# Optimization experiments

Measured on AMD Instinct MI355X. Metric: run time of the kernel, lower is better.

The kernel has to match this reference:

```python
import jax, jax.numpy as jnp
import numpy as np

BETA = 0.25


def setup_inputs() -> dict:
    key = jax.random.key(0)
    k1, k2 = jax.random.split(key)
    B, T, D, K = 16, 4096, 256, 4096
    z_e = jax.random.normal(k1, (B, T, D), dtype=jnp.float32)
    # emulate uniform(-1/K, 1/K) init but any values work for correctness
    codebook = jax.random.uniform(k2, (K, D), dtype=jnp.float32,
                                  minval=-1.0 / K, maxval=1.0 / K)
    return {"z_e": z_e, "codebook": codebook}


def reference(z_e, codebook):
    D = codebook.shape[1]
    z_flat = z_e.reshape(-1, D)                                  # [N, D]
    # squared L2 distances: ||z||^2 + ||e||^2 - 2 z.e
    z_norm = jnp.sum(z_flat ** 2, axis=1, keepdims=True)          # [N, 1]
    e_norm = jnp.sum(codebook ** 2, axis=1)                       # [K]
    dist = z_norm + e_norm - 2.0 * jnp.matmul(z_flat, codebook.T) # [N, K]
    idx_flat = jnp.argmin(dist, axis=1)                           # [N]
    idx = idx_flat.reshape(z_e.shape[:-1])                        # [B, T]
    z_q = codebook[idx]                                           # [B, T, D]
    # commitment loss: beta * mse(stop_grad(z_q), z_e)
    loss = BETA * jnp.mean((jax.lax.stop_gradient(z_q) - z_e) ** 2)
    # straight-through estimator
    z_q_st = z_e + jax.lax.stop_gradient(z_q - z_e)
    return z_q_st, idx, loss
```

## Files before the change

kernel.cpp:

```cpp
#include <hip/hip_runtime.h>
#include <cfloat>

#define NROWS 65536
#define DIM   256
#define KCB   4096

#define EPS_WIN  1.8e-4f
#define CAND_CAP 16
#define SROWS    64

typedef __attribute__((ext_vector_type(8))) short short8;
typedef __attribute__((ext_vector_type(4))) float f32x4;

__device__ inline unsigned short f2bf(float x) {
  unsigned int u = __float_as_uint(x);
  return (unsigned short)((u + 0x7fffu + ((u >> 16) & 1u)) >> 16);
}

__global__ void prep_norms_kernel(const float* __restrict__ z, const float* __restrict__ cb,
                                  unsigned short* __restrict__ zh, unsigned short* __restrict__ eh,
                                  float* __restrict__ znorm, float* __restrict__ enorm) {
  const int r    = blockIdx.x * 4 + (threadIdx.x >> 6);
  const int lane = threadIdx.x & 63;
  const float* src; unsigned short* dst; float* nrm; int row;
  if (r < NROWS) { src = z;  dst = zh; nrm = znorm; row = r; }
  else           { src = cb; dst = eh; nrm = enorm; row = r - NROWS; }
  const float4 v = ((const float4*)(src + (size_t)row * DIM))[lane];
  union { unsigned short us[4]; uint2 u2; } o;
  o.us[0] = f2bf(v.x); o.us[1] = f2bf(v.y); o.us[2] = f2bf(v.z); o.us[3] = f2bf(v.w);
  *(uint2*)(dst + (size_t)row * DIM + lane * 4) = o.u2;
  float s = v.x * v.x + v.y * v.y + v.z * v.z + v.w * v.w;
  #pragma unroll
  for (int off = 32; off > 0; off >>= 1) s += __shfl_down(s, off);
  if (lane == 0) nrm[row] = s;
}

__launch_bounds__(256, 3)
__global__ void screen_kernel(const unsigned short* __restrict__ zh,
                              const unsigned short* __restrict__ eh,
                              const float* __restrict__ enorm,
                              unsigned int* __restrict__ counts,
                              unsigned short* __restrict__ cands) {
  __shared__ __align__(16) unsigned short a_s[8][SROWS][32];
  __shared__ __align__(16) unsigned short b_s[2][128][32];
  __shared__ float tilemin_s[2][SROWS];
  __shared__ unsigned int cnt_s[SROWS];
  __shared__ unsigned short cand_s[SROWS * CAND_CAP];

  const int tid = threadIdx.x;
  const int wv  = tid >> 6;
  const int ln  = tid & 63;
  const int l15 = ln & 15;
  const int lg  = ln >> 4;
  const int wr  = wv >> 1;
  const int wc  = wv & 1;
  const int rbase = blockIdx.x * SROWS;

  if (tid < SROWS) cnt_s[tid] = 0u;

  {
    const unsigned short* abase = zh + (size_t)rbase * DIM;
    unsigned short* aflat = &a_s[0][0][0];
    #pragma unroll
    for (int i = 0; i < 8; ++i) {
      const int G  = i * 256 + tid;
      const int dc = G >> 8, rem = G & 255;
      const int c  = rem >> 2, sw = rem & 3;
      const int s4 = sw ^ ((c >> 1) & 3);
      __builtin_amdgcn_global_load_lds(
          (const uint4*)(abase + (size_t)c * 256 + dc * 32 + s4 * 8),
          (uint4*)(aflat + (size_t)G * 8), 16, 0, 0);
    }
  }

  float rm[8];
  #pragma unroll
  for (int s = 0; s < 8; ++s) rm[s] = FLT_MAX;

  unsigned short* bflat = &b_s[0][0][0];

  #pragma unroll 1
  for (int kt = 0; kt < KCB / 128; ++kt) {
    const int kcb0 = kt * 128;

    f32x4 acc[2][4];
    #pragma unroll
    for (int fr = 0; fr < 2; ++fr)
      #pragma unroll
      for (int fc = 0; fc < 4; ++fc)
        acc[fr][fc] = (f32x4){0.f, 0.f, 0.f, 0.f};

    #pragma unroll 1
    for (int ph = 0; ph < 4; ++ph) {
      __syncthreads();
      #pragma unroll
      for (int i = 0; i < 4; ++i) {
        const int G   = i * 256 + tid;
        const int dc2 = G >> 9, rem = G & 511;
        const int c   = rem >> 2, sw = rem & 3;
        const int s4  = sw ^ ((c >> 1) & 3);
        __builtin_amdgcn_global_load_lds(
            (const uint4*)(eh + (size_t)(kcb0 + c) * 256 + (ph * 2 + dc2) * 32 + s4 * 8),
            (uint4*)(bflat + (size_t)G * 8), 16, 0, 0);
      }
      __syncthreads();

      #pragma unroll
      for (int dc2 = 0; dc2 < 2; ++dc2) {
        const int dcg = ph * 2 + dc2;
        short8 af_[2];
        #pragma unroll
        for (int fr = 0; fr < 2; ++fr) {
          const int r  = wr * 32 + fr * 16 + l15;
          const int sl = lg ^ ((r >> 1) & 3);
          af_[fr] = *(const short8*)(&a_s[dcg][r][sl * 8]);
        }
        short8 bf[4];
        #pragma unroll
        for (int fc = 0; fc < 4; ++fc) {
          const int c  = wc * 64 + fc * 16 + l15;
          const int sw = lg ^ ((c >> 1) & 3);
          bf[fc] = *(const short8*)(&b_s[dc2][c][sw * 8]);
        }
        #pragma unroll
        for (int fr = 0; fr < 2; ++fr)
          #pragma unroll
          for (int fc = 0; fc < 4; ++fc)
            acc[fr][fc] = __builtin_amdgcn_mfma_f32_16x16x32_bf16(
                af_[fr], bf[fc], acc[fr][fc], 0, 0, 0);
      }
    }

    float en_[4];
    #pragma unroll
    for (int fc = 0; fc < 4; ++fc) en_[fc] = enorm[kcb0 + wc * 64 + fc * 16 + l15];

    float tm[8];
    #pragma unroll
    for (int s = 0; s < 8; ++s) tm[s] = FLT_MAX;

    #pragma unroll
    for (int fr = 0; fr < 2; ++fr)
      #pragma unroll
      for (int fc = 0; fc < 4; ++fc)
        #pragma unroll
        for (int q = 0; q < 4; ++q) {
          const float d_ = fmaf(-2.0f, acc[fr][fc][q], en_[fc]);
          tm[fr * 4 + q] = fminf(tm[fr * 4 + q], d_);
        }

    #pragma unroll
    for (int s = 0; s < 8; ++s) {
      float v = tm[s];
      v = fminf(v, __shfl_xor(v, 1));
      v = fminf(v, __shfl_xor(v, 2));
      v = fminf(v, __shfl_xor(v, 4));
      v = fminf(v, __shfl_xor(v, 8));
      if (l15 == 0)
        tilemin_s[wc][wr * 32 + (s >> 2) * 16 + lg * 4 + (s & 3)] = v;
    }
    __syncthreads();

    float gmin = FLT_MAX;
    #pragma unroll
    for (int s = 0; s < 8; ++s) {
      const int rl = wr * 32 + (s >> 2) * 16 + lg * 4 + (s & 3);
      const float comb = fminf(tilemin_s[0][rl], tilemin_s[1][rl]);
      const float m = fminf(rm[s], comb);
      rm[s] = m;
      gmin = fminf(gmin, tm[s] - m);
    }

    if (__any(gmin <= EPS_WIN)) {
      #pragma unroll
      for (int fr = 0; fr < 2; ++fr)
        #pragma unroll
        for (int fc = 0; fc < 4; ++fc)
          #pragma unroll
          for (int q = 0; q < 4; ++q) {
            const float d_ = fmaf(-2.0f, acc[fr][fc][q], en_[fc]);
            if (d_ <= rm[fr * 4 + q] + EPS_WIN) {
              const int rl = wr * 32 + fr * 16 + lg * 4 + q;
              const unsigned int pos = atomicAdd(&cnt_s[rl], 1u);
              if (pos < CAND_CAP)
                cand_s[rl * CAND_CAP + pos] =
                    (unsigned short)(kcb0 + wc * 64 + fc * 16 + l15);
            }
          }
    }
  }

  __syncthreads();
  if (tid < SROWS) counts[rbase + tid] = cnt_s[tid];
  for (int i = tid; i < SROWS * CAND_CAP; i += 256)
    cands[(size_t)rbase * CAND_CAP + i] = cand_s[i];
}

__global__ void rescore_kernel(const float* __restrict__ z, const float* __restrict__ cb,
                               const float* __restrict__ znorm, const float* __restrict__ enorm,
                               const unsigned int* __restrict__ counts,
                               const unsigned short* __restrict__ cands,
                               float* __restrict__ out_zq, float* __restrict__ out_idx,
                               float* __restrict__ partials) {
  const int gw  = (blockIdx.x * 256 + threadIdx.x) >> 6;
  const int ln  = threadIdx.x & 63;
  const int row = gw * 4 + (ln >> 4);
  const int ci  = ln & 15;
  const unsigned int cnt = counts[row];
  if (cnt > CAND_CAP) return;

  const int active = ci < (int)cnt;
  const int k = active ? (int)cands[(size_t)row * CAND_CAP + ci] : 0;
  const float4* zr4 = (const float4*)(z  + (size_t)row * DIM);
  const float4* er4 = (const float4*)(cb + (size_t)k   * DIM);
  float ax = 0.f, ay = 0.f, az = 0.f, aw = 0.f;
  #pragma unroll 4
  for (int d = 0; d < DIM / 4; ++d) {
    const float4 zv = zr4[d], ev = er4[d];
    ax = fmaf(zv.x, ev.x, ax); ay = fmaf(zv.y, ev.y, ay);
    az = fmaf(zv.z, ev.z, az); aw = fmaf(zv.w, ev.w, aw);
  }
  const float dot = (ax + ay) + (az + aw);
  const float dist = fmaf(-2.0f, dot, znorm[row] + enorm[k]);
  float bv = active ? dist : FLT_MAX;
  int   bk = active ? k : 0x7fffffff;
  #pragma unroll
  for (int off = 1; off < 16; off <<= 1) {
    const float ov = __shfl_xor(bv, off);
    const int   ok = __shfl_xor(bk, off);
    if (ov < bv || (ov == bv && ok < bk)) { bv = ov; bk = ok; }
  }
  const float4* br4 = (const float4*)(cb + (size_t)bk * DIM);
  float4* o4 = (float4*)(out_zq + (size_t)row * DIM);
  float sq = 0.0f;
  #pragma unroll
  for (int t = 0; t < 4; ++t) {
    const int p = ci + 16 * t;
    const float4 zv = zr4[p], ev = br4[p];
    float4 st;
    const float dx = ev.x - zv.x, dy = ev.y - zv.y, dz = ev.z - zv.z, dw = ev.w - zv.w;
    st.x = zv.x + dx; st.y = zv.y + dy; st.z = zv.z + dz; st.w = zv.w + dw;
    o4[p] = st;
    sq += dx * dx + dy * dy + dz * dz + dw * dw;
  }
  #pragma unroll
  for (int off = 1; off < 16; off <<= 1) sq += __shfl_xor(sq, off);
  if (ci == 0) { out_idx[row] = (float)bk; partials[row] = sq; }
}

__global__ void fallback_kernel(const float* __restrict__ z, const float* __restrict__ cb,
                                const float* __restrict__ znorm, const float* __restrict__ enorm,
                                const unsigned int* __restrict__ counts,
                                float* __restrict__ out_zq, float* __restrict__ out_idx,
                                float* __restrict__ partials) {
  __shared__ float bd_s[256];
  __shared__ int   bk_s[256];
  const int tid = threadIdx.x;
  for (int row = blockIdx.x; row < NROWS; row += gridDim.x) {
    if (counts[row] <= CAND_CAP) continue;
    const float zn = znorm[row];
    const float* zr = z + (size_t)row * DIM;
    float bv = FLT_MAX; int bk = 0x7fffffff;
    for (int k = tid; k < KCB; k += 256) {
      const float* er = cb + (size_t)k * DIM;
      float acc = 0.0f;
      #pragma unroll 8
      for (int d = 0; d < DIM; ++d) acc = fmaf(zr[d], er[d], acc);
      const float dist = fmaf(-2.0f, acc, zn + enorm[k]);
      if (dist < bv || (dist == bv && k < bk)) { bv = dist; bk = k; }
    }
    bd_s[tid] = bv; bk_s[tid] = bk;
    __syncthreads();
    for (int s = 128; s > 0; s >>= 1) {
      if (tid < s) {
        const float ov = bd_s[tid + s]; const int ok = bk_s[tid + s];
        if (ov < bd_s[tid] || (ov == bd_s[tid] && ok < bk_s[tid])) {
          bd_s[tid] = ov; bk_s[tid] = ok;
        }
      }
      __syncthreads();
    }
    const int kb = bk_s[0];
    const float zv = zr[tid];
    const float ev = cb[(size_t)kb * DIM + tid];
    const float dd = ev - zv;
    out_zq[(size_t)row * DIM + tid] = zv + dd;
    if (tid == 0) out_idx[row] = (float)kb;
    __syncthreads();
    bd_s[tid] = dd * dd;
    __syncthreads();
    for (int s = 128; s > 0; s >>= 1) {
      if (tid < s) bd_s[tid] += bd_s[tid + s];
      __syncthreads();
    }
    if (tid == 0) partials[row] = bd_s[0];
    __syncthreads();
  }
}

__global__ void loss_kernel(const float* __restrict__ partials, int n,
                            float* __restrict__ out_loss) {
  float s = 0.0f;
  for (int i = threadIdx.x; i < n; i += 256) s += partials[i];
  #pragma unroll
  for (int off = 32; off > 0; off >>= 1) s += __shfl_down(s, off);
  __shared__ float ps[4];
  if ((threadIdx.x & 63) == 0) ps[threadIdx.x >> 6] = s;
  __syncthreads();
  if (threadIdx.x == 0)
    *out_loss = 0.25f * (((ps[0] + ps[1]) + (ps[2] + ps[3])) *
                         (1.0f / (float)((size_t)NROWS * DIM)));
}

__global__ void norms_kernel(const float* __restrict__ x, float* __restrict__ out) {
  const int row  = blockIdx.x * 4 + (threadIdx.x >> 6);
  const int lane = threadIdx.x & 63;
  const float4 v = ((const float4*)(x + (size_t)row * DIM))[lane];
  float s = v.x * v.x + v.y * v.y + v.z * v.z + v.w * v.w;
  #pragma unroll
  for (int off = 32; off > 0; off >>= 1) s += __shfl_down(s, off);
  if (lane == 0) out[row] = s;
}

#define BM 128
#define BK 128
#define BD 32
#define LSTR 36
__launch_bounds__(256, 2)
__global__ void argmin_kernel(const float* __restrict__ z,
                              const float* __restrict__ cb,
                              const float* __restrict__ znorm,
                              const float* __restrict__ enorm,
                              int* __restrict__ idx_out) {
  __shared__ float z_s[BM * LSTR];
  __shared__ float e_s[BK * LSTR];
  __shared__ float zn_s[BM];
  const int tid = threadIdx.x;
  const int tx = tid & 15;
  const int ty = tid >> 4;
  const int rbase = blockIdx.x * BM;
  if (tid < BM) zn_s[tid] = znorm[rbase + tid];
  float bestv[8]; int besti[8];
  #pragma unroll
  for (int i = 0; i < 8; ++i) { bestv[i] = FLT_MAX; besti[i] = 0; }
  for (int kc = 0; kc < KCB; kc += BK) {
    float acc[8][8];
    #pragma unroll
    for (int i = 0; i < 8; ++i)
      #pragma unroll
      for (int j = 0; j < 8; ++j) acc[i][j] = 0.0f;
    for (int dc = 0; dc < DIM; dc += BD) {
      __syncthreads();
      #pragma unroll
      for (int p = 0; p < 4; ++p) {
        const int el = p * 256 + tid;
        const int r  = el >> 3;
        const int c4 = (el & 7) * 4;
        *(float4*)(&z_s[r * LSTR + c4]) =
            *(const float4*)(z + (size_t)(rbase + r) * DIM + dc + c4);
        *(float4*)(&e_s[r * LSTR + c4]) =
            *(const float4*)(cb + (size_t)(kc + r) * DIM + dc + c4);
      }
      __syncthreads();
      #pragma unroll 1
      for (int dd = 0; dd < BD; dd += 4) {
        float4 b[8];
        #pragma unroll
        for (int j = 0; j < 8; ++j)
          b[j] = *(const float4*)(&e_s[(tx + 16 * j) * LSTR + dd]);
        #pragma unroll
        for (int i = 0; i < 8; ++i) {
          const float4 a = *(const float4*)(&z_s[(ty + 16 * i) * LSTR + dd]);
          #pragma unroll
          for (int j = 0; j < 8; ++j)
            acc[i][j] += a.x * b[j].x + a.y * b[j].y + a.z * b[j].z + a.w * b[j].w;
        }
      }
    }
    float en[8];
    #pragma unroll
    for (int j = 0; j < 8; ++j) en[j] = enorm[kc + tx + 16 * j];
    #pragma unroll
    for (int i = 0; i < 8; ++i) {
      const float zn = zn_s[ty + 16 * i];
      #pragma unroll
      for (int j = 0; j < 8; ++j) {
        const float t1 = zn + en[j];
        const float dist = t1 - 2.0f * acc[i][j];
        const int k = kc + tx + 16 * j;
        if (dist < bestv[i]) { bestv[i] = dist; besti[i] = k; }
      }
    }
  }
  #pragma unroll
  for (int i = 0; i < 8; ++i) {
    float lv = bestv[i]; int li = besti[i];
    #pragma unroll
    for (int off = 1; off < 16; off <<= 1) {
      const float ov = __shfl_xor(lv, off);
      const int   oi = __shfl_xor(li, off);
      if (ov < lv || (ov == lv && oi < li)) { lv = ov; li = oi; }
    }
    if (tx == 0) idx_out[rbase + ty + 16 * i] = li;
  }
}

__global__ void gather_kernel(const float* __restrict__ z,
                              const float* __restrict__ cb,
                              const int* __restrict__ idx,
                              float* __restrict__ out_zq,
                              float* __restrict__ out_idx,
                              float* __restrict__ partials) {
  const int row  = blockIdx.x * 4 + (threadIdx.x >> 6);
  const int lane = threadIdx.x & 63;
  const int k = idx[row];
  const float4 zv = ((const float4*)(z  + (size_t)row * DIM))[lane];
  const float4 ev = ((const float4*)(cb + (size_t)k   * DIM))[lane];
  float4 d, st;
  d.x = ev.x - zv.x; d.y = ev.y - zv.y; d.z = ev.z - zv.z; d.w = ev.w - zv.w;
  st.x = zv.x + d.x; st.y = zv.y + d.y; st.z = zv.z + d.z; st.w = zv.w + d.w;
  ((float4*)(out_zq + (size_t)row * DIM))[lane] = st;
  if (lane == 0) out_idx[row] = (float)k;
  float s = d.x * d.x + d.y * d.y + d.z * d.z + d.w * d.w;
  #pragma unroll
  for (int off = 32; off > 0; off >>= 1) s += __shfl_down(s, off);
  __shared__ float ps[4];
  if (lane == 0) ps[threadIdx.x >> 6] = s;
  __syncthreads();
  if (threadIdx.x == 0)
    partials[blockIdx.x] = (ps[0] + ps[1]) + (ps[2] + ps[3]);
}

extern "C" void kernel_launch(void* const* d_in, const int* in_sizes, int n_in,
                              void* d_out, int out_size, void* d_ws, size_t ws_size,
                              hipStream_t stream) {
  const float* z  = (const float*)d_in[0];
  const float* cb = (const float*)d_in[1];

  float* out_zq   = (float*)d_out;
  float* out_idx  = out_zq + (size_t)NROWS * DIM;
  float* out_loss = out_idx + NROWS;

  char* w = (char*)d_ws;
  unsigned short* zh    = (unsigned short*)(w);
  unsigned short* eh    = (unsigned short*)(w + 33554432);
  float* enorm          = (float*)(w + 35651584);
  float* znorm          = (float*)(w + 35667968);
  unsigned int* counts  = (unsigned int*)(w + 36192256);
  unsigned short* cands = (unsigned short*)(w + 36454400);
  float* partials       = (float*)(w + 38551552);
  const size_t NEED = 38813696;

  if (ws_size >= NEED) {
    hipLaunchKernelGGL(prep_norms_kernel, dim3((NROWS + KCB) / 4), dim3(256), 0, stream,
                       z, cb, zh, eh, znorm, enorm);
    hipLaunchKernelGGL(screen_kernel, dim3(NROWS / SROWS), dim3(256), 0, stream,
                       zh, eh, enorm, counts, cands);
    hipLaunchKernelGGL(rescore_kernel, dim3(NROWS / 16), dim3(256), 0, stream,
                       z, cb, znorm, enorm, counts, cands, out_zq, out_idx, partials);
    hipLaunchKernelGGL(fallback_kernel, dim3(256), dim3(256), 0, stream,
                       z, cb, znorm, enorm, counts, out_zq, out_idx, partials);
    hipLaunchKernelGGL(loss_kernel, dim3(1), dim3(256), 0, stream,
                       partials, NROWS, out_loss);
  } else {
    float* ws         = (float*)d_ws;
    float* enorm_l    = ws;
    float* znorm_l    = ws + KCB;
    int*   idx_l      = (int*)(ws + KCB + NROWS);
    float* partials_l = ws + KCB + 2 * NROWS;
    hipLaunchKernelGGL(norms_kernel, dim3(KCB / 4), dim3(256), 0, stream, cb, enorm_l);
    hipLaunchKernelGGL(norms_kernel, dim3(NROWS / 4), dim3(256), 0, stream, z, znorm_l);
    hipLaunchKernelGGL(argmin_kernel, dim3(NROWS / BM), dim3(256), 0, stream,
                       z, cb, znorm_l, enorm_l, idx_l);
    hipLaunchKernelGGL(gather_kernel, dim3(NROWS / 4), dim3(256), 0, stream,
                       z, cb, idx_l, out_zq, out_idx, partials_l);
    hipLaunchKernelGGL(loss_kernel, dim3(1), dim3(256), 0, stream,
                       partials_l, NROWS / 4, out_loss);
  }
}
```

Before: 563.3 us.

## Double-buffer codebook tiles and give each wave full tile width

The screen kernel now double-buffers the codebook B tile in LDS. The next 32-dim chunk is prefetched with global_load_lds while MFMAs run on the current one, so there is one barrier per chunk instead of two per phase. Waves are remapped so each owns 16 rows across all 128 codebook columns, which removes the cross-wave shared-memory tile-min exchange and its extra barrier. In exchange, each wave reuses its A fragment across more B reads and issues more LDS reads of B per MFMA. The prefetch also wraps around and issues one redundant load at the end.

```diff
diff --git a/kernel.cpp b/kernel.cpp
--- a/kernel.cpp
+++ b/kernel.cpp
@@ -43,7 +43,6 @@
                               unsigned short* __restrict__ cands) {
   __shared__ __align__(16) unsigned short a_s[8][SROWS][32];
   __shared__ __align__(16) unsigned short b_s[2][128][32];
-  __shared__ float tilemin_s[2][SROWS];
   __shared__ unsigned int cnt_s[SROWS];
   __shared__ unsigned short cand_s[SROWS * CAND_CAP];
 
@@ -52,8 +51,6 @@
   const int ln  = tid & 63;
   const int l15 = ln & 15;
   const int lg  = ln >> 4;
-  const int wr  = wv >> 1;
-  const int wc  = wv & 1;
   const int rbase = blockIdx.x * SROWS;
 
   if (tid < SROWS) cnt_s[tid] = 0u;
@@ -71,122 +68,113 @@
           (const uint4*)(abase + (size_t)c * 256 + dc * 32 + s4 * 8),
           (uint4*)(aflat + (size_t)G * 8), 16, 0, 0);
     }
-  }
-
-  float rm[8];
-  #pragma unroll
-  for (int s = 0; s < 8; ++s) rm[s] = FLT_MAX;
-
-  unsigned short* bflat = &b_s[0][0][0];
+    unsigned short* b0 = &b_s[0][0][0];
+    #pragma unroll
+    for (int i = 0; i < 2; ++i) {
+      const int G  = i * 256 + tid;
+      const int c  = G >> 2, sw = G & 3;
+      const int s4 = sw ^ ((c >> 1) & 3);
+      __builtin_amdgcn_global_load_lds(
+          (const uint4*)(eh + (size_t)c * 256 + s4 * 8),
+          (uint4*)(b0 + (size_t)G * 8), 16, 0, 0);
+    }
+  }
+  __syncthreads();
+
+  const int ar = l15;
+  const int arow = wv * 16 + ar;
+  const int asl = lg ^ ((arow >> 1) & 3);
+
+  float rm[4];
+  #pragma unroll
+  for (int q = 0; q < 4; ++q) rm[q] = FLT_MAX;
+
+  int cur = 0;
 
   #pragma unroll 1
   for (int kt = 0; kt < KCB / 128; ++kt) {
     const int kcb0 = kt * 128;
 
-    f32x4 acc[2][4];
-    #pragma unroll
-    for (int fr = 0; fr < 2; ++fr)
-      #pragma unroll
-      for (int fc = 0; fc < 4; ++fc)
-        acc[fr][fc] = (f32x4){0.f, 0.f, 0.f, 0.f};
+    f32x4 acc[8];
+    #pragma unroll
+    for (int fc = 0; fc < 8; ++fc) acc[fc] = (f32x4){0.f, 0.f, 0.f, 0.f};
 
     #pragma unroll 1
-    for (int ph = 0; ph < 4; ++ph) {
+    for (int dc = 0; dc < 8; ++dc) {
+      {
+        const int t   = (kt * 8 + dc + 1) & 255;
+        const int nkt = t >> 3, ndc = t & 7;
+        unsigned short* bn = &b_s[cur ^ 1][0][0];
+        #pragma unroll
+        for (int i = 0; i < 2; ++i) {
+          const int G  = i * 256 + tid;
+          const int c  = G >> 2, sw = G & 3;
+          const int s4 = sw ^ ((c >> 1) & 3);
+          __builtin_amdgcn_global_load_lds(
+              (const uint4*)(eh + (size_t)(nkt * 128 + c) * 256 + ndc * 32 + s4 * 8),
+              (uint4*)(bn + (size_t)G * 8), 16, 0, 0);
+        }
+      }
+
+      const short8 af = *(const short8*)(&a_s[dc][arow][asl * 8]);
+      short8 bf[8];
+      #pragma unroll
+      for (int fc = 0; fc < 8; ++fc) {
+        const int c  = fc * 16 + l15;
+        const int sw = lg ^ ((c >> 1) & 3);
+        bf[fc] = *(const short8*)(&b_s[cur][c][sw * 8]);
+      }
+      #pragma unroll
+      for (int fc = 0; fc < 8; ++fc)
+        acc[fc] = __builtin_amdgcn_mfma_f32_16x16x32_bf16(af, bf[fc], acc[fc], 0, 0, 0);
+
       __syncthreads();
-      #pragma unroll
-      for (int i = 0; i < 4; ++i) {
-        const int G   = i * 256 + tid;
-        const int dc2 = G >> 9, rem = G & 511;
-        const int c   = rem >> 2, sw = rem & 3;
-        const int s4  = sw ^ ((c >> 1) & 3);
-        __builtin_amdgcn_global_load_lds(
-            (const uint4*)(eh + (size_t)(kcb0 + c) * 256 + (ph * 2 + dc2) * 32 + s4 * 8),
-            (uint4*)(bflat + (size_t)G * 8), 16, 0, 0);
-      }
-      __syncthreads();
-
-      #pragma unroll
-      for (int dc2 = 0; dc2 < 2; ++dc2) {
-        const int dcg = ph * 2 + dc2;
-        short8 af_[2];
-        #pragma unroll
-        for (int fr = 0; fr < 2; ++fr) {
-          const int r  = wr * 32 + fr * 16 + l15;
-          const int sl = lg ^ ((r >> 1) & 3);
-          af_[fr] = *(const short8*)(&a_s[dcg][r][sl * 8]);
-        }
-        short8 bf[4];
-        #pragma unroll
-        for (int fc = 0; fc < 4; ++fc) {
-          const int c  = wc * 64 + fc * 16 + l15;
-          const int sw = lg ^ ((c >> 1) & 3);
-          bf[fc] = *(const short8*)(&b_s[dc2][c][sw * 8]);
-        }
-        #pragma unroll
-        for (int fr = 0; fr < 2; ++fr)
-          #pragma unroll
-          for (int fc = 0; fc < 4; ++fc)
-            acc[fr][fc] = __builtin_amdgcn_mfma_f32_16x16x32_bf16(
-                af_[fr], bf[fc], acc[fr][fc], 0, 0, 0);
-      }
-    }
-
-    float en_[4];
-    #pragma unroll
-    for (int fc = 0; fc < 4; ++fc) en_[fc] = enorm[kcb0 + wc * 64 + fc * 16 + l15];
-
-    float tm[8];
-    #pragma unroll
-    for (int s = 0; s < 8; ++s) tm[s] = FLT_MAX;
-
-    #pragma unroll
-    for (int fr = 0; fr < 2; ++fr)
-      #pragma unroll
-      for (int fc = 0; fc < 4; ++fc)
-        #pragma unroll
-        for (int q = 0; q < 4; ++q) {
-          const float d_ = fmaf(-2.0f, acc[fr][fc][q], en_[fc]);
-          tm[fr * 4 + q] = fminf(tm[fr * 4 + q], d_);
-        }
-
-    #pragma unroll
-    for (int s = 0; s < 8; ++s) {
-      float v = tm[s];
+      cur ^= 1;
+    }
+
+    float en_[8];
+    #pragma unroll
+    for (int fc = 0; fc < 8; ++fc) en_[fc] = enorm[kcb0 + fc * 16 + l15];
+
+    float tm[4];
+    #pragma unroll
+    for (int q = 0; q < 4; ++q) tm[q] = FLT_MAX;
+
+    #pragma unroll
+    for (int fc = 0; fc < 8; ++fc)
+      #pragma unroll
+      for (int q = 0; q < 4; ++q) {
+        const float d_ = fmaf(-2.0f, acc[fc][q], en_[fc]);
+        tm[q] = fminf(tm[q], d_);
+      }
+
+    float gmin = FLT_MAX;
+    #pragma unroll
+    for (int q = 0; q < 4; ++q) {
+      float v = tm[q];
       v = fminf(v, __shfl_xor(v, 1));
       v = fminf(v, __shfl_xor(v, 2));
       v = fminf(v, __shfl_xor(v, 4));
       v = fminf(v, __shfl_xor(v, 8));
-      if (l15 == 0)
-        tilemin_s[wc][wr * 32 + (s >> 2) * 16 + lg * 4 + (s & 3)] = v;
-    }
-    __syncthreads();
-
-    float gmin = FLT_MAX;
-    #pragma unroll
-    for (int s = 0; s < 8; ++s) {
-      const int rl = wr * 32 + (s >> 2) * 16 + lg * 4 + (s & 3);
-      const float comb = fminf(tilemin_s[0][rl], tilemin_s[1][rl]);
-      const float m = fminf(rm[s], comb);
-      rm[s] = m;
-      gmin = fminf(gmin, tm[s] - m);
+      const float m = fminf(rm[q], v);
+      rm[q] = m;
+      gmin = fminf(gmin, tm[q] - m);
     }
 
     if (__any(gmin <= EPS_WIN)) {
       #pragma unroll
-      for (int fr = 0; fr < 2; ++fr)
+      for (int fc = 0; fc < 8; ++fc)
         #pragma unroll
-        for (int fc = 0; fc < 4; ++fc)
-          #pragma unroll
-          for (int q = 0; q < 4; ++q) {
-            const float d_ = fmaf(-2.0f, acc[fr][fc][q], en_[fc]);
-            if (d_ <= rm[fr * 4 + q] + EPS_WIN) {
-              const int rl = wr * 32 + fr * 16 + lg * 4 + q;
-              const unsigned int pos = atomicAdd(&cnt_s[rl], 1u);
-              if (pos < CAND_CAP)
-                cand_s[rl * CAND_CAP + pos] =
-                    (unsigned short)(kcb0 + wc * 64 + fc * 16 + l15);
-            }
+        for (int q = 0; q < 4; ++q) {
+          const float d_ = fmaf(-2.0f, acc[fc][q], en_[fc]);
+          if (d_ <= rm[q] + EPS_WIN) {
+            const int rl = wv * 16 + lg * 4 + q;
+            const unsigned int pos = atomicAdd(&cnt_s[rl], 1u);
+            if (pos < CAND_CAP)
+              cand_s[rl * CAND_CAP + pos] =
+                  (unsigned short)(kcb0 + fc * 16 + l15);
           }
+        }
     }
   }
 
```

New measurement: 547.2 us. -2.9%, faster.
